# Performance work log

Measured on AMD Instinct MI355X. Metric: run time of the kernel, lower is better.

## Reference

```python
import jax, jax.numpy as jnp
import numpy as np


def setup_inputs() -> dict:
    key = jax.random.key(0)
    k1, k2 = jax.random.split(key)
    B, H, Lq, Lk, D = 4, 8, 2048, 2048, 64
    input1 = jax.random.normal(k1, (B, H, Lq, D), dtype=jnp.float32)   # query [B,H,Lq,d]
    input2 = jax.random.normal(k2, (B, H, D, Lk), dtype=jnp.float32)   # key   [B,H,d,Lk]
    return {"input1": input1, "input2": input2}


def reference(input1, input2):
    # out[b,h,i,j] = sum_c (q[b,h,i,c] - k[b,h,c,j])**2
    # Expanded: ||q_i||^2 + ||k_j||^2 - 2 q_i . k_j  (avoids [B,H,Lq,Lk,d] blowup)
    q2 = jnp.sum(input1 * input1, axis=-1)[..., :, None]   # [B,H,Lq,1]
    k2 = jnp.sum(input2 * input2, axis=-2)[..., None, :]   # [B,H,1,Lk]
    qk = jnp.einsum("bhid,bhdj->bhij", input1, input2)     # [B,H,Lq,Lk]
    return q2 + k2 - 2.0 * qk
```

## Files before the change

### kernel.cpp

```cpp
#include <hip/hip_runtime.h>
#include <hip/hip_bf16.h>


#define BH 32
#define LQ 2048
#define LK 2048
#define DD 64
#define TM 128
#define TN 128
#define LDA 72
#define LDB 130

typedef __attribute__((ext_vector_type(8))) short short8;
typedef __attribute__((ext_vector_type(4))) float f32x4;

__device__ __forceinline__ unsigned short f2bf(float f) {
  unsigned u = __builtin_bit_cast(unsigned, f);
  u += 0x7fffu + ((u >> 16) & 1u);
  return (unsigned short)(u >> 16);
}

__device__ __forceinline__ float bflo(unsigned w) {
  return __builtin_bit_cast(float, w << 16);
}
__device__ __forceinline__ float bfhi(unsigned w) {
  return __builtin_bit_cast(float, w & 0xffff0000u);
}

__global__ __launch_bounds__(256) void sg_kernel(const float* __restrict__ Q,
                                                 const float* __restrict__ K,
                                                 float* __restrict__ out) {
  __shared__ __align__(16) unsigned short As[TM * LDA];
  __shared__ __align__(16) unsigned short Bs[DD * LDB];
  __shared__ float q2s[TM];
  __shared__ float k2s[TN];

  const int bh  = blockIdx.z;
  const int gm0 = blockIdx.y * TM;
  const int gn0 = blockIdx.x * TN;
  const int tid = threadIdx.x;

  {
    int row  = tid >> 1;
    int half = tid & 1;
    const float4* src = (const float4*)(Q + ((size_t)bh * LQ + gm0 + row) * DD + half * 32);
#pragma unroll
    for (int g = 0; g < 4; ++g) {
      float4 a = src[2 * g];
      float4 b = src[2 * g + 1];
      int4 pk;
      pk.x = (int)((unsigned)f2bf(a.x) | ((unsigned)f2bf(a.y) << 16));
      pk.y = (int)((unsigned)f2bf(a.z) | ((unsigned)f2bf(a.w) << 16));
      pk.z = (int)((unsigned)f2bf(b.x) | ((unsigned)f2bf(b.y) << 16));
      pk.w = (int)((unsigned)f2bf(b.z) | ((unsigned)f2bf(b.w) << 16));
      *(int4*)&As[row * LDA + half * 32 + g * 8] = pk;
    }
  }

  {
    int jl = (tid & 31) * 4;
#pragma unroll
    for (int it = 0; it < 8; ++it) {
      int c = it * 8 + (tid >> 5);
      float4 v = *(const float4*)(K + ((size_t)bh * DD + c) * LK + gn0 + jl);
      unsigned lo = (unsigned)f2bf(v.x) | ((unsigned)f2bf(v.y) << 16);
      unsigned hi = (unsigned)f2bf(v.z) | ((unsigned)f2bf(v.w) << 16);
      *(unsigned*)&Bs[c * LDB + jl]     = lo;
      *(unsigned*)&Bs[c * LDB + jl + 2] = hi;
    }
  }

  __syncthreads();

  if (tid < TM) {
    float s = 0.f;
#pragma unroll
    for (int ch = 0; ch < 8; ++ch) {
      int4 pk = *(const int4*)&As[tid * LDA + ch * 8];
      float v;
      v = bflo((unsigned)pk.x); s += v * v; v = bfhi((unsigned)pk.x); s += v * v;
      v = bflo((unsigned)pk.y); s += v * v; v = bfhi((unsigned)pk.y); s += v * v;
      v = bflo((unsigned)pk.z); s += v * v; v = bfhi((unsigned)pk.z); s += v * v;
      v = bflo((unsigned)pk.w); s += v * v; v = bfhi((unsigned)pk.w); s += v * v;
    }
    q2s[tid] = s;
  } else if (tid < 192) {
    int j0 = (tid - 128) * 2;
    float s0 = 0.f, s1 = 0.f;
#pragma unroll
    for (int c = 0; c < DD; ++c) {
      unsigned w = *(const unsigned*)&Bs[c * LDB + j0];
      float v0 = bflo(w), v1 = bfhi(w);
      s0 += v0 * v0;
      s1 += v1 * v1;
    }
    k2s[j0] = s0;
    k2s[j0 + 1] = s1;
  }

  __syncthreads();

  const int wave = tid >> 6;
  const int lane = tid & 63;
  const int wm   = (wave >> 1) * 64;
  const int wn   = (wave & 1) * 64;
  const int n15  = lane & 15;
  const int qd   = lane >> 4;

  f32x4 acc[4][4];
#pragma unroll
  for (int mi = 0; mi < 4; ++mi)
#pragma unroll
    for (int ni = 0; ni < 4; ++ni)
      acc[mi][ni] = (f32x4){0.f, 0.f, 0.f, 0.f};

#pragma unroll
  for (int kk = 0; kk < DD; kk += 32) {
    short8 a[4], b[4];
#pragma unroll
    for (int mi = 0; mi < 4; ++mi)
      a[mi] = *(const short8*)&As[(wm + mi * 16 + n15) * LDA + kk + qd * 8];
#pragma unroll
    for (int ni = 0; ni < 4; ++ni) {
      __align__(16) unsigned short tmp[8];
#pragma unroll
      for (int jj = 0; jj < 8; ++jj)
        tmp[jj] = Bs[(kk + qd * 8 + jj) * LDB + wn + ni * 16 + n15];
      b[ni] = *(short8*)tmp;
    }
#pragma unroll
    for (int mi = 0; mi < 4; ++mi)
#pragma unroll
      for (int ni = 0; ni < 4; ++ni)
        acc[mi][ni] = __builtin_amdgcn_mfma_f32_16x16x32_bf16(a[mi], b[ni], acc[mi][ni], 0, 0, 0);
  }

  const size_t obase = ((size_t)bh * LQ + gm0) * (size_t)LK + gn0;
#pragma unroll
  for (int mi = 0; mi < 4; ++mi) {
#pragma unroll
    for (int ni = 0; ni < 4; ++ni) {
      float k2v = k2s[wn + ni * 16 + n15];
#pragma unroll
      for (int r = 0; r < 4; ++r) {
        int lrow = wm + mi * 16 + qd * 4 + r;
        float v = q2s[lrow] + k2v - 2.0f * acc[mi][ni][r];
        out[obase + (size_t)lrow * LK + (size_t)(wn + ni * 16 + n15)] = v;
      }
    }
  }
}

extern "C" void kernel_launch(void* const* d_in, const int* in_sizes, int n_in,
                              void* d_out, int out_size, void* d_ws, size_t ws_size,
                              hipStream_t stream) {
  const float* Q = (const float*)d_in[0];
  const float* K = (const float*)d_in[1];
  float* out = (float*)d_out;
  dim3 grid(LK / TN, LQ / TM, BH);
  sg_kernel<<<grid, 256, 0, stream>>>(Q, K, out);
}
```

Baseline: 626.5 us.

## Transpose K tile in LDS and stage output through shared memory for vector stores

K is now loaded column-wise and stored transposed in LDS, so the MFMA B operands become single 16-byte vector reads instead of eight scalar gathers. Both norm computations are unified to one per thread over the contiguous tiles, which removes a barrier. The epilogue writes results into LDS in two halves and then emits coalesced float4 global stores. The cost is uncoalesced scalar global loads of K, extra barriers in the epilogue, and reuse of LDS with launch_bounds set for 4 blocks.

```diff
diff --git a/kernel.cpp b/kernel.cpp
--- a/kernel.cpp
+++ b/kernel.cpp
@@ -8,32 +8,28 @@
 #define DD 64
 #define TM 128
 #define TN 128
-#define LDA 72
-#define LDB 130
+#define LDT 72
+#define SST 136
 
 typedef __attribute__((ext_vector_type(8))) short short8;
 typedef __attribute__((ext_vector_type(4))) float f32x4;
 
-__device__ __forceinline__ unsigned short f2bf(float f) {
+__device__ __forceinline__ unsigned f2bf(float f) {
   unsigned u = __builtin_bit_cast(unsigned, f);
   u += 0x7fffu + ((u >> 16) & 1u);
-  return (unsigned short)(u >> 16);
+  return u >> 16;
 }
+__device__ __forceinline__ float bflo(unsigned w) { return __builtin_bit_cast(float, w << 16); }
+__device__ __forceinline__ float bfhi(unsigned w) { return __builtin_bit_cast(float, w & 0xffff0000u); }
 
-__device__ __forceinline__ float bflo(unsigned w) {
-  return __builtin_bit_cast(float, w << 16);
-}
-__device__ __forceinline__ float bfhi(unsigned w) {
-  return __builtin_bit_cast(float, w & 0xffff0000u);
-}
+__global__ __launch_bounds__(256, 4) void sg_kernel(const float* __restrict__ Q,
+                                                    const float* __restrict__ K,
+                                                    float* __restrict__ out) {
+  __shared__ __align__(16) unsigned short smem[2 * TM * LDT];
+  __shared__ float norms[256];
 
-__global__ __launch_bounds__(256) void sg_kernel(const float* __restrict__ Q,
-                                                 const float* __restrict__ K,
-                                                 float* __restrict__ out) {
-  __shared__ __align__(16) unsigned short As[TM * LDA];
-  __shared__ __align__(16) unsigned short Bs[DD * LDB];
-  __shared__ float q2s[TM];
-  __shared__ float k2s[TN];
+  unsigned short* As = smem;
+  unsigned short* Bt = smem + TM * LDT;
 
   const int bh  = blockIdx.z;
   const int gm0 = blockIdx.y * TM;
@@ -41,64 +37,55 @@
   const int tid = threadIdx.x;
 
   {
-    int row  = tid >> 1;
-    int half = tid & 1;
-    const float4* src = (const float4*)(Q + ((size_t)bh * LQ + gm0 + row) * DD + half * 32);
+    const float* qbase = Q + ((size_t)bh * LQ + gm0) * DD;
 #pragma unroll
-    for (int g = 0; g < 4; ++g) {
-      float4 a = src[2 * g];
-      float4 b = src[2 * g + 1];
+    for (int it = 0; it < 4; ++it) {
+      int c = it * 256 + tid;
+      const float4* p = (const float4*)(qbase + c * 8);
+      float4 a = p[0];
+      float4 b = p[1];
       int4 pk;
-      pk.x = (int)((unsigned)f2bf(a.x) | ((unsigned)f2bf(a.y) << 16));
-      pk.y = (int)((unsigned)f2bf(a.z) | ((unsigned)f2bf(a.w) << 16));
-      pk.z = (int)((unsigned)f2bf(b.x) | ((unsigned)f2bf(b.y) << 16));
-      pk.w = (int)((unsigned)f2bf(b.z) | ((unsigned)f2bf(b.w) << 16));
-      *(int4*)&As[row * LDA + half * 32 + g * 8] = pk;
+      pk.x = (int)(f2bf(a.x) | (f2bf(a.y) << 16));
+      pk.y = (int)(f2bf(a.z) | (f2bf(a.w) << 16));
+      pk.z = (int)(f2bf(b.x) | (f2bf(b.y) << 16));
+      pk.w = (int)(f2bf(b.z) | (f2bf(b.w) << 16));
+      *(int4*)&As[(c >> 3) * LDT + (c & 7) * 8] = pk;
     }
   }
 
   {
-    int jl = (tid & 31) * 4;
+    int col = tid & 127;
+    int c0b = (tid >> 7) * 32;
+    const float* kp = K + (size_t)bh * DD * LK + gn0 + col;
 #pragma unroll
     for (int it = 0; it < 8; ++it) {
-      int c = it * 8 + (tid >> 5);
-      float4 v = *(const float4*)(K + ((size_t)bh * DD + c) * LK + gn0 + jl);
-      unsigned lo = (unsigned)f2bf(v.x) | ((unsigned)f2bf(v.y) << 16);
-      unsigned hi = (unsigned)f2bf(v.z) | ((unsigned)f2bf(v.w) << 16);
-      *(unsigned*)&Bs[c * LDB + jl]     = lo;
-      *(unsigned*)&Bs[c * LDB + jl + 2] = hi;
+      int c0 = c0b + it * 4;
+      float v0 = kp[(size_t)(c0 + 0) * LK];
+      float v1 = kp[(size_t)(c0 + 1) * LK];
+      float v2 = kp[(size_t)(c0 + 2) * LK];
+      float v3 = kp[(size_t)(c0 + 3) * LK];
+      uint2 w;
+      w.x = f2bf(v0) | (f2bf(v1) << 16);
+      w.y = f2bf(v2) | (f2bf(v3) << 16);
+      *(uint2*)&Bt[col * LDT + c0] = w;
     }
   }
 
   __syncthreads();
 
-  if (tid < TM) {
+  {
     float s = 0.f;
 #pragma unroll
     for (int ch = 0; ch < 8; ++ch) {
-      int4 pk = *(const int4*)&As[tid * LDA + ch * 8];
+      int4 pk = *(const int4*)&smem[tid * LDT + ch * 8];
       float v;
       v = bflo((unsigned)pk.x); s += v * v; v = bfhi((unsigned)pk.x); s += v * v;
       v = bflo((unsigned)pk.y); s += v * v; v = bfhi((unsigned)pk.y); s += v * v;
       v = bflo((unsigned)pk.z); s += v * v; v = bfhi((unsigned)pk.z); s += v * v;
       v = bflo((unsigned)pk.w); s += v * v; v = bfhi((unsigned)pk.w); s += v * v;
     }
-    q2s[tid] = s;
-  } else if (tid < 192) {
-    int j0 = (tid - 128) * 2;
-    float s0 = 0.f, s1 = 0.f;
-#pragma unroll
-    for (int c = 0; c < DD; ++c) {
-      unsigned w = *(const unsigned*)&Bs[c * LDB + j0];
-      float v0 = bflo(w), v1 = bfhi(w);
-      s0 += v0 * v0;
-      s1 += v1 * v1;
-    }
-    k2s[j0] = s0;
-    k2s[j0 + 1] = s1;
+    norms[tid] = s;
   }
-
-  __syncthreads();
 
   const int wave = tid >> 6;
   const int lane = tid & 63;
@@ -119,15 +106,10 @@
     short8 a[4], b[4];
 #pragma unroll
     for (int mi = 0; mi < 4; ++mi)
-      a[mi] = *(const short8*)&As[(wm + mi * 16 + n15) * LDA + kk + qd * 8];
+      a[mi] = *(const short8*)&As[(wm + mi * 16 + n15) * LDT + kk + qd * 8];
 #pragma unroll
-    for (int ni = 0; ni < 4; ++ni) {
-      __align__(16) unsigned short tmp[8];
-#pragma unroll
-      for (int jj = 0; jj < 8; ++jj)
-        tmp[jj] = Bs[(kk + qd * 8 + jj) * LDB + wn + ni * 16 + n15];
-      b[ni] = *(short8*)tmp;
-    }
+    for (int ni = 0; ni < 4; ++ni)
+      b[ni] = *(const short8*)&Bt[(wn + ni * 16 + n15) * LDT + kk + qd * 8];
 #pragma unroll
     for (int mi = 0; mi < 4; ++mi)
 #pragma unroll
@@ -135,18 +117,34 @@
         acc[mi][ni] = __builtin_amdgcn_mfma_f32_16x16x32_bf16(a[mi], b[ni], acc[mi][ni], 0, 0, 0);
   }
 
+  float* sf = (float*)smem;
   const size_t obase = ((size_t)bh * LQ + gm0) * (size_t)LK + gn0;
+
+  for (int h = 0; h < 2; ++h) {
+    __syncthreads();
+    if ((wave >> 1) == h) {
 #pragma unroll
-  for (int mi = 0; mi < 4; ++mi) {
+      for (int mi = 0; mi < 4; ++mi) {
 #pragma unroll
-    for (int ni = 0; ni < 4; ++ni) {
-      float k2v = k2s[wn + ni * 16 + n15];
+        for (int ni = 0; ni < 4; ++ni) {
+          float k2v = norms[128 + wn + ni * 16 + n15];
 #pragma unroll
-      for (int r = 0; r < 4; ++r) {
-        int lrow = wm + mi * 16 + qd * 4 + r;
-        float v = q2s[lrow] + k2v - 2.0f * acc[mi][ni][r];
-        out[obase + (size_t)lrow * LK + (size_t)(wn + ni * 16 + n15)] = v;
+          for (int r = 0; r < 4; ++r) {
+            int lr = mi * 16 + qd * 4 + r;
+            sf[lr * SST + wn + ni * 16 + n15] =
+                norms[h * 64 + lr] + k2v - 2.0f * acc[mi][ni][r];
+          }
+        }
       }
+    }
+    __syncthreads();
+    int rr = tid >> 5;
+    int cc = (tid & 31) * 4;
+#pragma unroll
+    for (int it = 0; it < 8; ++it) {
+      int row = it * 8 + rr;
+      float4 v = *(const float4*)&sf[row * SST + cc];
+      *(float4*)&out[obase + (size_t)(h * 64 + row) * LK + cc] = v;
     }
   }
 }
```

Result: faster. 562.2 us (-10.3%).
